# Optimization experiments

Hardware: AMD Instinct MI355X
Metric: run time of the kernel (lower is better)

The kernel has to match this reference:

```python
import jax, jax.numpy as jnp
import numpy as np
from jax import lax

N_QUBITS = 4   # in_channels * kernel_size^2 = 1*2*2
N_LAYERS = 2
K = 2
STRIDE = 1


def _bshape(theta, N):
    # broadcast scalar or (N,) angle to (N, 1, 1, ..., 1) for statevector broadcasting
    return jnp.broadcast_to(theta, (N,)).reshape((N,) + (1,) * N_QUBITS)


def _rx(state, theta, w):
    # RX(theta) on wire w (axis w+1): cos(t/2) I - i sin(t/2) X
    N = state.shape[0]
    c = _bshape(jnp.cos(theta * 0.5), N)
    s = _bshape(jnp.sin(theta * 0.5), N)
    return c * state - 1j * s * jnp.flip(state, axis=w + 1)


def _rz(state, theta, w):
    # RZ(theta): phase e^{-i t/2} on |0>, e^{+i t/2} on |1> of wire w
    N = state.shape[0]
    sgn = jnp.array([-0.5, 0.5], dtype=state.real.dtype).reshape(
        (1,) * (w + 1) + (2,) + (1,) * (N_QUBITS - 1 - w))
    return state * jnp.exp(1j * (_bshape(theta, N) * sgn))


def _cnot(state, control, target):
    ca, ta = control + 1, target + 1
    s0 = jnp.take(state, 0, axis=ca)
    s1 = jnp.take(state, 1, axis=ca)
    ta2 = ta if ta < ca else ta - 1
    s1 = jnp.flip(s1, axis=ta2)
    return jnp.stack([s0, s1], axis=ca)


def _simulate(angles, params):
    # angles: (N, n_qubits) float32; params: (n_layers, n_qubits, 2)
    N = angles.shape[0]
    state = jnp.zeros((N,) + (2,) * N_QUBITS, dtype=jnp.complex64)
    state = state.at[(slice(None),) + (0,) * N_QUBITS].set(1.0)
    # AngleEmbedding: RX(x_w) on wire w
    for w in range(N_QUBITS):
        state = _rx(state, angles[:, w], w)
    # quantum_circuit_1
    for l in range(N_LAYERS):
        for w in range(N_QUBITS):
            state = _rx(state, params[l, w, 0], w)
            state = _rz(state, params[l, w, 1], w)
        for w in range(N_QUBITS - 1):
            # qml.CNOT(wires=[w+1, w]) -> control w+1, target w
            state = _cnot(state, w + 1, w)
    probs = state.real ** 2 + state.imag ** 2  # (N, 2,...,2)
    zs = []
    for w in range(N_QUBITS):
        other = tuple(a for a in range(1, N_QUBITS + 1) if a != w + 1)
        m = probs.sum(axis=other)  # (N, 2)
        zs.append(m[:, 0] - m[:, 1])
    return jnp.stack(zs, axis=1)  # (N, n_qubits)


def _forward(x, params):
    B, C, H, W = x.shape
    Ho = (H - K) // STRIDE + 1
    Wo = (W - K) // STRIDE + 1
    # (B, C*K*K, Ho, Wo); feature dim flattened channel-major (C, kh, kw),
    # matching torch.flatten(input[:, :, i:i+k, j:j+k], start_dim=1)
    patches = lax.conv_general_dilated_patches(x, (K, K), (STRIDE, STRIDE), 'VALID')
    angles = patches.transpose(0, 2, 3, 1).reshape(-1, N_QUBITS)  # (B*Ho*Wo, nq)
    z = _simulate(angles, params)  # (B*Ho*Wo, nq)
    return z.reshape(B, Ho, Wo, N_QUBITS).transpose(0, 3, 1, 2)  # (B, nq, Ho, Wo)


def setup_inputs() -> dict:
    key = jax.random.key(0)
    k1, k2 = jax.random.split(key)
    x = jax.random.uniform(k1, (32, 1, 128, 128), dtype=jnp.float32)
    params = jax.random.uniform(k2, (N_LAYERS, N_QUBITS, 2), dtype=jnp.float32)
    return {"x": x, "params": params}


def reference(x, params):
    return _forward(x, params)
```

## Files before the change

kernel.cpp:

```cpp
#include <hip/hip_runtime.h>


#define HH 128
#define WW 128
#define HO 127
#define WO 127
#define BB 32
#define JSLOTS 32

template <int M>
__device__ __forceinline__ void rx_gate(float* re, float* im, float th) {
    float s, c;
    __sincosf(th * 0.5f, &s, &c);
#pragma unroll
    for (int idx = 0; idx < 16; ++idx) {
        if (idx & M) continue;
        const int p = idx | M;
        float r0 = re[idx], i0 = im[idx], r1 = re[p], i1 = im[p];
        re[idx] = fmaf(c, r0, s * i1);
        im[idx] = fmaf(c, i0, -s * r1);
        re[p]   = fmaf(c, r1, s * i0);
        im[p]   = fmaf(c, i1, -s * r0);
    }
}

template <int M>
__device__ __forceinline__ void rz_gate(float* re, float* im, float th) {
    float sp, cp;
    __sincosf(th * 0.5f, &sp, &cp);
#pragma unroll
    for (int idx = 0; idx < 16; ++idx) {
        float r = re[idx], q = im[idx];
        if (idx & M) {
            re[idx] = fmaf(r, cp, -q * sp);
            im[idx] = fmaf(q, cp, r * sp);
        } else {
            re[idx] = fmaf(r, cp, q * sp);
            im[idx] = fmaf(q, cp, -r * sp);
        }
    }
}

template <int CM, int TM>
__device__ __forceinline__ void cnot_gate(float* re, float* im) {
#pragma unroll
    for (int idx = 0; idx < 16; ++idx) {
        if ((idx & CM) && !(idx & TM)) {
            const int p = idx | TM;
            float t;
            t = re[idx]; re[idx] = re[p]; re[p] = t;
            t = im[idx]; im[idx] = im[p]; im[p] = t;
        }
    }
}

__device__ __forceinline__ void param_circuit(float* re, float* im,
                                              const float* __restrict__ prm) {
#pragma unroll
    for (int l = 0; l < 2; ++l) {
        const float* p = prm + l * 8;
        rx_gate<8>(re, im, p[0]); rz_gate<8>(re, im, p[1]);
        rx_gate<4>(re, im, p[2]); rz_gate<4>(re, im, p[3]);
        rx_gate<2>(re, im, p[4]); rz_gate<2>(re, im, p[5]);
        rx_gate<1>(re, im, p[6]); rz_gate<1>(re, im, p[7]);
        cnot_gate<4, 8>(re, im);
        cnot_gate<2, 4>(re, im);
        cnot_gate<1, 2>(re, im);
    }
}

__global__ __launch_bounds__(256) void qconv_fused(
    const float* __restrict__ x, const float* __restrict__ prm,
    float* __restrict__ out) {
    __shared__ float Ur[16][16];
    __shared__ float Ui[16][16];
    __shared__ float Mr[4][16][16];
    __shared__ float Mi[4][16][16];
    __shared__ float4 sW[81];

    const int tid = threadIdx.x;

    if (tid < 16) {
        float re[16], im[16];
#pragma unroll
        for (int k = 0; k < 16; ++k) { re[k] = (k == tid) ? 1.f : 0.f; im[k] = 0.f; }
        param_circuit(re, im, prm);
#pragma unroll
        for (int k = 0; k < 16; ++k) { Ur[k][tid] = re[k]; Ui[k][tid] = im[k]; }
    }
    __syncthreads();

    {
        const int w = tid >> 6;
        const int zbit = 8 >> w;
        const int base = (tid & 63) * 4;
#pragma unroll
        for (int r = 0; r < 4; ++r) {
            const int e = base + r;
            const int j = e >> 4, i = e & 15;
            float sr = 0.f, si = 0.f;
            for (int k = 0; k < 16; ++k) {
                float zk = (k & zbit) ? -1.f : 1.f;
                float ar = Ur[k][j], ai = Ui[k][j];
                float br = Ur[k][i], bi = Ui[k][i];
                sr += zk * fmaf(ar, br, ai * bi);
                si += zk * fmaf(ar, bi, -ai * br);
            }
            Mr[w][j][i] = sr;
            Mi[w][j][i] = si;
        }
    }
    __syncthreads();

    for (int cc = tid; cc < 324; cc += 256) {
        const int w = cc / 81;
        int p = cc % 81;
        const int pidx = p;
        const int t3 = p % 3; p /= 3;
        const int t2 = p % 3; p /= 3;
        const int t1 = p % 3;
        const int t0 = p / 3;
        const int f = (t0 == 1 ? 8 : 0) | (t1 == 1 ? 4 : 0) |
                      (t2 == 1 ? 2 : 0) | (t3 == 1 ? 1 : 0);
        float acc = 0.f;
        for (int i = 0; i < 16; ++i) {
            float pr = 1.f, pi = 0.f;
            int ib;
            ib = (i >> 3) & 1;
            if (t0 == 2) { if (ib) { pr = -pr; pi = -pi; } }
            else if (t0 == 1) { float tt = pr; if (ib) { pr = -pi; pi = tt; } else { pr = pi; pi = -tt; } }
            ib = (i >> 2) & 1;
            if (t1 == 2) { if (ib) { pr = -pr; pi = -pi; } }
            else if (t1 == 1) { float tt = pr; if (ib) { pr = -pi; pi = tt; } else { pr = pi; pi = -tt; } }
            ib = (i >> 1) & 1;
            if (t2 == 2) { if (ib) { pr = -pr; pi = -pi; } }
            else if (t2 == 1) { float tt = pr; if (ib) { pr = -pi; pi = tt; } else { pr = pi; pi = -tt; } }
            ib = i & 1;
            if (t3 == 2) { if (ib) { pr = -pr; pi = -pi; } }
            else if (t3 == 1) { float tt = pr; if (ib) { pr = -pi; pi = tt; } else { pr = pi; pi = -tt; } }
            const int j = i ^ f;
            acc += pr * Mr[w][j][i] - pi * Mi[w][j][i];
        }
        ((float*)sW)[pidx * 4 + w] = acc * (1.0f / 16.0f);
    }
    __syncthreads();

    const int tid_g = blockIdx.x * blockDim.x + tid;
    const int slot = tid_g % JSLOTS;
    int t = tid_g / JSLOTS;
    const int i = t % HO;
    const int b = t / HO;
    const int j0 = slot * 4;

    const float* row0 = x + ((size_t)b * HH + i) * WW + j0;
    const float* row1 = row0 + WW;
    const float4 v0 = *(const float4*)row0;
    const float4 v1 = *(const float4*)row1;
    const bool has5 = (j0 + 4 < WW);
    const float x04 = has5 ? row0[4] : 0.f;
    const float x14 = has5 ? row1[4] : 0.f;
    const float r0[5] = {v0.x, v0.y, v0.z, v0.w, x04};
    const float r1[5] = {v1.x, v1.y, v1.z, v1.w, x14};

    float t0v[4][3], t1v[4][3], t2v[4][3], t3v[4][3];
#pragma unroll
    for (int pp = 0; pp < 4; ++pp) {
        float s, c;
        __sincosf(r0[pp], &s, &c);     t0v[pp][0] = 1.f; t0v[pp][1] = -s; t0v[pp][2] = c;
        __sincosf(r0[pp + 1], &s, &c); t1v[pp][0] = 1.f; t1v[pp][1] = -s; t1v[pp][2] = c;
        __sincosf(r1[pp], &s, &c);     t2v[pp][0] = 1.f; t2v[pp][1] = -s; t2v[pp][2] = c;
        __sincosf(r1[pp + 1], &s, &c); t3v[pp][0] = 1.f; t3v[pp][1] = -s; t3v[pp][2] = c;
    }

    float acc[4][4];
#pragma unroll
    for (int pp = 0; pp < 4; ++pp)
#pragma unroll
        for (int w = 0; w < 4; ++w) acc[pp][w] = 0.f;

#pragma unroll
    for (int p0 = 0; p0 < 3; ++p0) {
        float g0[4];
#pragma unroll
        for (int pp = 0; pp < 4; ++pp) g0[pp] = t0v[pp][p0];
#pragma unroll
        for (int p1 = 0; p1 < 3; ++p1) {
            float g1[4];
#pragma unroll
            for (int pp = 0; pp < 4; ++pp) g1[pp] = g0[pp] * t1v[pp][p1];
#pragma unroll
            for (int p2 = 0; p2 < 3; ++p2) {
                float g2[4];
#pragma unroll
                for (int pp = 0; pp < 4; ++pp) g2[pp] = g1[pp] * t2v[pp][p2];
#pragma unroll
                for (int p3 = 0; p3 < 3; ++p3) {
                    const int p = ((p0 * 3 + p1) * 3 + p2) * 3 + p3;
                    const float4 q = sW[p];
#pragma unroll
                    for (int pp = 0; pp < 4; ++pp) {
                        const float g = g2[pp] * t3v[pp][p3];
                        acc[pp][0] = fmaf(g, q.x, acc[pp][0]);
                        acc[pp][1] = fmaf(g, q.y, acc[pp][1]);
                        acc[pp][2] = fmaf(g, q.z, acc[pp][2]);
                        acc[pp][3] = fmaf(g, q.w, acc[pp][3]);
                    }
                }
            }
        }
    }

    const int npatch = (j0 + 4 <= WO) ? 4 : (WO - j0);
    float* obase = out + (((size_t)b * 4) * HO + (size_t)i) * WO + j0;
#pragma unroll
    for (int w = 0; w < 4; ++w) {
        float* o = obase + (size_t)w * HO * WO;
        for (int pp = 0; pp < npatch; ++pp) o[pp] = acc[pp][w];
    }
}

extern "C" void kernel_launch(void* const* d_in, const int* in_sizes, int n_in,
                              void* d_out, int out_size, void* d_ws, size_t ws_size,
                              hipStream_t stream) {
    const float* x = (const float*)d_in[0];
    const float* prm = (const float*)d_in[1];
    float* out = (float*)d_out;

    const int total_threads = BB * HO * JSLOTS;
    const int blocks = total_threads / 256;
    qconv_fused<<<blocks, 256, 0, stream>>>(x, prm, out);
}
```

Baseline: 70.70 us.

## Parallelize per-block unitary build with shuffles, halve M work, share sincos, use 512-thread blocks

The 16x16 circuit unitary is now built by 64 threads, each holding 4 amplitudes, with wavefront shuffles for cross-lane gates, instead of 16 serial threads with 16-element states. The Z-observable matrices are computed as I - 2*(sum over the Z=-1 half), which halves the inner loop, and they are stored in padded shared arrays to avoid bank conflicts. The per-pixel sincos calls drop from 16 to 10 by sharing overlapping patch columns. Blocks grow to 512 threads so the redundant per-block setup is paid half as often, at the cost of fewer resident blocks and larger scheduling granularity.

```diff
diff --git a/kernel.cpp b/kernel.cpp
--- a/kernel.cpp
+++ b/kernel.cpp
@@ -7,114 +7,120 @@
 #define WO 127
 #define BB 32
 #define JSLOTS 32
-
-template <int M>
-__device__ __forceinline__ void rx_gate(float* re, float* im, float th) {
-    float s, c;
-    __sincosf(th * 0.5f, &s, &c);
-#pragma unroll
-    for (int idx = 0; idx < 16; ++idx) {
-        if (idx & M) continue;
-        const int p = idx | M;
-        float r0 = re[idx], i0 = im[idx], r1 = re[p], i1 = im[p];
-        re[idx] = fmaf(c, r0, s * i1);
-        im[idx] = fmaf(c, i0, -s * r1);
-        re[p]   = fmaf(c, r1, s * i0);
-        im[p]   = fmaf(c, i1, -s * r0);
-    }
-}
-
-template <int M>
-__device__ __forceinline__ void rz_gate(float* re, float* im, float th) {
-    float sp, cp;
-    __sincosf(th * 0.5f, &sp, &cp);
-#pragma unroll
-    for (int idx = 0; idx < 16; ++idx) {
-        float r = re[idx], q = im[idx];
-        if (idx & M) {
-            re[idx] = fmaf(r, cp, -q * sp);
-            im[idx] = fmaf(q, cp, r * sp);
-        } else {
-            re[idx] = fmaf(r, cp, q * sp);
-            im[idx] = fmaf(q, cp, -r * sp);
-        }
-    }
-}
-
-template <int CM, int TM>
-__device__ __forceinline__ void cnot_gate(float* re, float* im) {
-#pragma unroll
-    for (int idx = 0; idx < 16; ++idx) {
-        if ((idx & CM) && !(idx & TM)) {
-            const int p = idx | TM;
-            float t;
-            t = re[idx]; re[idx] = re[p]; re[p] = t;
-            t = im[idx]; im[idx] = im[p]; im[p] = t;
-        }
-    }
-}
-
-__device__ __forceinline__ void param_circuit(float* re, float* im,
-                                              const float* __restrict__ prm) {
-#pragma unroll
-    for (int l = 0; l < 2; ++l) {
-        const float* p = prm + l * 8;
-        rx_gate<8>(re, im, p[0]); rz_gate<8>(re, im, p[1]);
-        rx_gate<4>(re, im, p[2]); rz_gate<4>(re, im, p[3]);
-        rx_gate<2>(re, im, p[4]); rz_gate<2>(re, im, p[5]);
-        rx_gate<1>(re, im, p[6]); rz_gate<1>(re, im, p[7]);
-        cnot_gate<4, 8>(re, im);
-        cnot_gate<2, 4>(re, im);
-        cnot_gate<1, 2>(re, im);
-    }
-}
-
-__global__ __launch_bounds__(256) void qconv_fused(
+#define TPB 512
+
+__global__ __launch_bounds__(TPB) void qconv_fused(
     const float* __restrict__ x, const float* __restrict__ prm,
     float* __restrict__ out) {
-    __shared__ float Ur[16][16];
-    __shared__ float Ui[16][16];
-    __shared__ float Mr[4][16][16];
-    __shared__ float Mi[4][16][16];
+    __shared__ float Utr[16][20];
+    __shared__ float Uti[16][20];
+    __shared__ float Mr[4][16][17];
+    __shared__ float Mi[4][16][17];
     __shared__ float4 sW[81];
 
     const int tid = threadIdx.x;
 
-    if (tid < 16) {
-        float re[16], im[16];
-#pragma unroll
-        for (int k = 0; k < 16; ++k) { re[k] = (k == tid) ? 1.f : 0.f; im[k] = 0.f; }
-        param_circuit(re, im, prm);
-#pragma unroll
-        for (int k = 0; k < 16; ++k) { Ur[k][tid] = re[k]; Ui[k][tid] = im[k]; }
+    if (tid < 64) {
+        const int c = tid >> 2;
+        const int g = tid & 3;
+        float re[4], im[4];
+#pragma unroll
+        for (int m = 0; m < 4; ++m) { re[m] = (4 * g + m == c) ? 1.f : 0.f; im[m] = 0.f; }
+
+#pragma unroll
+        for (int l = 0; l < 2; ++l) {
+            const float* p = prm + l * 8;
+            { float s, cc; __sincosf(p[0] * 0.5f, &s, &cc);
+              float pr[4], pi[4];
+#pragma unroll
+              for (int m = 0; m < 4; ++m) { pr[m] = __shfl_xor(re[m], 2); pi[m] = __shfl_xor(im[m], 2); }
+#pragma unroll
+              for (int m = 0; m < 4; ++m) { re[m] = fmaf(cc, re[m], s * pi[m]); im[m] = fmaf(cc, im[m], -s * pr[m]); } }
+            { float sp, cp; __sincosf(p[1] * 0.5f, &sp, &cp);
+              const float sg = (g & 2) ? sp : -sp;
+#pragma unroll
+              for (int m = 0; m < 4; ++m) { float r = re[m], q = im[m];
+                  re[m] = fmaf(r, cp, -q * sg); im[m] = fmaf(q, cp, r * sg); } }
+            { float s, cc; __sincosf(p[2] * 0.5f, &s, &cc);
+              float pr[4], pi[4];
+#pragma unroll
+              for (int m = 0; m < 4; ++m) { pr[m] = __shfl_xor(re[m], 1); pi[m] = __shfl_xor(im[m], 1); }
+#pragma unroll
+              for (int m = 0; m < 4; ++m) { re[m] = fmaf(cc, re[m], s * pi[m]); im[m] = fmaf(cc, im[m], -s * pr[m]); } }
+            { float sp, cp; __sincosf(p[3] * 0.5f, &sp, &cp);
+              const float sg = (g & 1) ? sp : -sp;
+#pragma unroll
+              for (int m = 0; m < 4; ++m) { float r = re[m], q = im[m];
+                  re[m] = fmaf(r, cp, -q * sg); im[m] = fmaf(q, cp, r * sg); } }
+            { float s, cc; __sincosf(p[4] * 0.5f, &s, &cc);
+              float r0 = re[0], r1 = re[1], r2 = re[2], r3 = re[3];
+              float i0 = im[0], i1 = im[1], i2 = im[2], i3 = im[3];
+              re[0] = fmaf(cc, r0, s * i2); im[0] = fmaf(cc, i0, -s * r2);
+              re[1] = fmaf(cc, r1, s * i3); im[1] = fmaf(cc, i1, -s * r3);
+              re[2] = fmaf(cc, r2, s * i0); im[2] = fmaf(cc, i2, -s * r0);
+              re[3] = fmaf(cc, r3, s * i1); im[3] = fmaf(cc, i3, -s * r1); }
+            { float sp, cp; __sincosf(p[5] * 0.5f, &sp, &cp);
+              float r, q;
+              r = re[0]; q = im[0]; re[0] = fmaf(r, cp,  q * sp); im[0] = fmaf(q, cp, -r * sp);
+              r = re[1]; q = im[1]; re[1] = fmaf(r, cp,  q * sp); im[1] = fmaf(q, cp, -r * sp);
+              r = re[2]; q = im[2]; re[2] = fmaf(r, cp, -q * sp); im[2] = fmaf(q, cp,  r * sp);
+              r = re[3]; q = im[3]; re[3] = fmaf(r, cp, -q * sp); im[3] = fmaf(q, cp,  r * sp); }
+            { float s, cc; __sincosf(p[6] * 0.5f, &s, &cc);
+              float r0 = re[0], r1 = re[1], r2 = re[2], r3 = re[3];
+              float i0 = im[0], i1 = im[1], i2 = im[2], i3 = im[3];
+              re[0] = fmaf(cc, r0, s * i1); im[0] = fmaf(cc, i0, -s * r1);
+              re[1] = fmaf(cc, r1, s * i0); im[1] = fmaf(cc, i1, -s * r0);
+              re[2] = fmaf(cc, r2, s * i3); im[2] = fmaf(cc, i2, -s * r3);
+              re[3] = fmaf(cc, r3, s * i2); im[3] = fmaf(cc, i3, -s * r2); }
+            { float sp, cp; __sincosf(p[7] * 0.5f, &sp, &cp);
+              float r, q;
+              r = re[0]; q = im[0]; re[0] = fmaf(r, cp,  q * sp); im[0] = fmaf(q, cp, -r * sp);
+              r = re[1]; q = im[1]; re[1] = fmaf(r, cp, -q * sp); im[1] = fmaf(q, cp,  r * sp);
+              r = re[2]; q = im[2]; re[2] = fmaf(r, cp,  q * sp); im[2] = fmaf(q, cp, -r * sp);
+              r = re[3]; q = im[3]; re[3] = fmaf(r, cp, -q * sp); im[3] = fmaf(q, cp,  r * sp); }
+#pragma unroll
+            for (int m = 0; m < 4; ++m) {
+                float pr = __shfl_xor(re[m], 2), pi = __shfl_xor(im[m], 2);
+                if (g & 1) { re[m] = pr; im[m] = pi; }
+            }
+            re[2] = __shfl_xor(re[2], 1); im[2] = __shfl_xor(im[2], 1);
+            re[3] = __shfl_xor(re[3], 1); im[3] = __shfl_xor(im[3], 1);
+            { float t;
+              t = re[1]; re[1] = re[3]; re[3] = t;
+              t = im[1]; im[1] = im[3]; im[3] = t; }
+        }
+        *(float4*)&Utr[c][4 * g] = make_float4(re[0], re[1], re[2], re[3]);
+        *(float4*)&Uti[c][4 * g] = make_float4(im[0], im[1], im[2], im[3]);
     }
     __syncthreads();
 
     {
-        const int w = tid >> 6;
+        const int e0 = tid * 2;
+        const int w = e0 >> 8;
+        const int j = (e0 >> 4) & 15;
+        const int i0 = e0 & 15;
         const int zbit = 8 >> w;
-        const int base = (tid & 63) * 4;
-#pragma unroll
-        for (int r = 0; r < 4; ++r) {
-            const int e = base + r;
-            const int j = e >> 4, i = e & 15;
-            float sr = 0.f, si = 0.f;
-            for (int k = 0; k < 16; ++k) {
-                float zk = (k & zbit) ? -1.f : 1.f;
-                float ar = Ur[k][j], ai = Ui[k][j];
-                float br = Ur[k][i], bi = Ui[k][i];
-                sr += zk * fmaf(ar, br, ai * bi);
-                si += zk * fmaf(ar, bi, -ai * br);
-            }
-            Mr[w][j][i] = sr;
-            Mi[w][j][i] = si;
-        }
+        const int lowmask = zbit - 1;
+        float sr0 = 0.f, si0 = 0.f, sr1 = 0.f, si1 = 0.f;
+#pragma unroll
+        for (int t = 0; t < 8; ++t) {
+            const int k = ((t & ~lowmask) << 1) | zbit | (t & lowmask);
+            const float ar = Utr[j][k],      ai = Uti[j][k];
+            const float br0 = Utr[i0][k],    bi0 = Uti[i0][k];
+            const float br1 = Utr[i0 + 1][k], bi1 = Uti[i0 + 1][k];
+            sr0 += fmaf(ar, br0, ai * bi0);  si0 += fmaf(ar, bi0, -ai * br0);
+            sr1 += fmaf(ar, br1, ai * bi1);  si1 += fmaf(ar, bi1, -ai * br1);
+        }
+        Mr[w][j][i0]     = ((j == i0)     ? 1.f : 0.f) - 2.f * sr0;
+        Mi[w][j][i0]     = -2.f * si0;
+        Mr[w][j][i0 + 1] = ((j == i0 + 1) ? 1.f : 0.f) - 2.f * sr1;
+        Mi[w][j][i0 + 1] = -2.f * si1;
     }
     __syncthreads();
 
-    for (int cc = tid; cc < 324; cc += 256) {
-        const int w = cc / 81;
-        int p = cc % 81;
+    if (tid < 324) {
+        const int w = tid / 81;
+        int p = tid % 81;
         const int pidx = p;
         const int t3 = p % 3; p /= 3;
         const int t2 = p % 3; p /= 3;
@@ -145,7 +151,7 @@
     }
     __syncthreads();
 
-    const int tid_g = blockIdx.x * blockDim.x + tid;
+    const int tid_g = blockIdx.x * TPB + tid;
     const int slot = tid_g % JSLOTS;
     int t = tid_g / JSLOTS;
     const int i = t % HO;
@@ -162,14 +168,19 @@
     const float r0[5] = {v0.x, v0.y, v0.z, v0.w, x04};
     const float r1[5] = {v1.x, v1.y, v1.z, v1.w, x14};
 
+    float s0[5], c0[5], s1[5], c1[5];
+#pragma unroll
+    for (int u = 0; u < 5; ++u) {
+        __sincosf(r0[u], &s0[u], &c0[u]);
+        __sincosf(r1[u], &s1[u], &c1[u]);
+    }
     float t0v[4][3], t1v[4][3], t2v[4][3], t3v[4][3];
 #pragma unroll
     for (int pp = 0; pp < 4; ++pp) {
-        float s, c;
-        __sincosf(r0[pp], &s, &c);     t0v[pp][0] = 1.f; t0v[pp][1] = -s; t0v[pp][2] = c;
-        __sincosf(r0[pp + 1], &s, &c); t1v[pp][0] = 1.f; t1v[pp][1] = -s; t1v[pp][2] = c;
-        __sincosf(r1[pp], &s, &c);     t2v[pp][0] = 1.f; t2v[pp][1] = -s; t2v[pp][2] = c;
-        __sincosf(r1[pp + 1], &s, &c); t3v[pp][0] = 1.f; t3v[pp][1] = -s; t3v[pp][2] = c;
+        t0v[pp][0] = 1.f; t0v[pp][1] = -s0[pp];     t0v[pp][2] = c0[pp];
+        t1v[pp][0] = 1.f; t1v[pp][1] = -s0[pp + 1]; t1v[pp][2] = c0[pp + 1];
+        t2v[pp][0] = 1.f; t2v[pp][1] = -s1[pp];     t2v[pp][2] = c1[pp];
+        t3v[pp][0] = 1.f; t3v[pp][1] = -s1[pp + 1]; t3v[pp][2] = c1[pp + 1];
     }
 
     float acc[4][4];
@@ -227,6 +238,6 @@
     float* out = (float*)d_out;
 
     const int total_threads = BB * HO * JSLOTS;
-    const int blocks = total_threads / 256;
-    qconv_fused<<<blocks, 256, 0, stream>>>(x, prm, out);
+    const int blocks = total_threads / TPB;
+    qconv_fused<<<blocks, TPB, 0, stream>>>(x, prm, out);
 }
```

Result: faster. 66.28 us (-6.3%).
